# Optimization experiments

Hardware: AMD Instinct MI355X
Metric: run time of the kernel (lower is better)

Reference implementation:

```python
import jax, jax.numpy as jnp
import numpy as np

N = 100000      # nodes
E = 1600000     # edges (before self-loops)
IN_DIM = 32
HID = 64        # per-head channels of conv1
H1 = 2          # heads of conv1
OUT = 64        # conv2 out channels, heads=1
LN_EPS = 1e-5
NEG_SLOPE = 0.2   # PyG GATConv default LeakyReLU slope


def setup_inputs() -> dict:
    key = jax.random.key(0)
    ks = jax.random.split(key, 13)
    g = lambda k, shape, sc=0.1: (jax.random.normal(k, shape, jnp.float32) * sc)
    return {
        "x": jax.random.normal(ks[0], (N, IN_DIM), jnp.float32),
        "edge_index": jax.random.randint(ks[1], (2, E), 0, N, dtype=jnp.int32),
        # conv1: heads=2, out=HID -> lin weight [IN_DIM, H1*HID], att [H1, HID]
        "W1": g(ks[2], (IN_DIM, H1 * HID)),
        "att_src1": g(ks[3], (H1, HID)),
        "att_dst1": g(ks[4], (H1, HID)),
        "bias1": jnp.zeros((H1 * HID,), jnp.float32),
        # LayerNorm over 128 features
        "gamma": jnp.ones((H1 * HID,), jnp.float32),
        "beta": jnp.zeros((H1 * HID,), jnp.float32),
        # conv2: heads=1, in=128, out=OUT
        "W2": g(ks[5], (H1 * HID, OUT)),
        "att_src2": g(ks[6], (1, OUT)),
        "att_dst2": g(ks[7], (1, OUT)),
        "bias2": jnp.zeros((OUT,), jnp.float32),
    }


def gat_layer(x, src, dst, W, att_src, att_dst, bias, heads, out_ch, n):
    """PyG GATConv (shared src/dst lin, add_self_loops handled by caller)."""
    h = (x @ W).reshape(n, heads, out_ch)                 # [N,H,C]
    a_s = jnp.einsum('nhc,hc->nh', h, att_src)            # [N,H]
    a_d = jnp.einsum('nhc,hc->nh', h, att_dst)
    e = jax.nn.leaky_relu(a_s[src] + a_d[dst], NEG_SLOPE) # [E,H]
    # segment softmax over incoming edges of each destination node
    emax = jax.ops.segment_max(e, dst, num_segments=n)    # [N,H]
    e = jnp.exp(e - emax[dst])
    esum = jax.ops.segment_sum(e, dst, num_segments=n)
    alpha = e / (esum[dst] + 1e-16)                       # [E,H]
    msg = h[src] * alpha[:, :, None]                      # [E,H,C]
    out = jax.ops.segment_sum(msg, dst, num_segments=n)   # [N,H,C]
    return out.reshape(n, heads * out_ch) + bias


def reference(x, edge_index, W1, att_src1, att_dst1, bias1, gamma, beta,
              W2, att_src2, att_dst2, bias2):
    n = x.shape[0]
    loops = jnp.arange(n, dtype=edge_index.dtype)
    src = jnp.concatenate([edge_index[0], loops])         # add self-loops
    dst = jnp.concatenate([edge_index[1], loops])

    h = gat_layer(x, src, dst, W1, att_src1, att_dst1, bias1, H1, HID, n)
    # LayerNorm over feature dim, then ReLU
    mu = h.mean(-1, keepdims=True)
    var = ((h - mu) ** 2).mean(-1, keepdims=True)
    h = (h - mu) * jax.lax.rsqrt(var + LN_EPS) * gamma + beta
    h = jax.nn.relu(h)

    return gat_layer(h, src, dst, W2, att_src2, att_dst2, bias2, 1, OUT, n)
```

## Files before the change

kernel.cpp:

```cpp
#include <hip/hip_runtime.h>
#include <hip/hip_bf16.h>
#include <hip/hip_fp16.h>

#define IN_DIM 32
#define HID 64
#define H1 2
#define F1 (H1 * HID)
#define OUT_CH 64
#define NEG_SLOPE 0.2f
#define LN_EPS 1e-5f

#define BSHIFT 9
#define BMASK ((1 << BSHIFT) - 1)
#define CHUNK 4096

typedef __attribute__((ext_vector_type(8))) short short8x;
typedef __attribute__((ext_vector_type(4))) float floatx4;

__device__ __forceinline__ float leaky(float x) {
    return x > 0.f ? x : NEG_SLOPE * x;
}
__device__ __forceinline__ float bf2f(__hip_bfloat16 v) { return __bfloat162float(v); }
__device__ __forceinline__ short f2bs(float v) {
    __hip_bfloat16 t = __float2bfloat16(v);
    return *reinterpret_cast<short*>(&t);
}
__device__ __forceinline__ float unpack_w(unsigned u, int hshift) {
    return __half2float(__ushort_as_half((unsigned short)(u >> hshift)));
}


__global__ __launch_bounds__(256) void k_bhist(const int* __restrict__ dst, int E, int nb,
                                               int* __restrict__ bcnt) {
    __shared__ int h[512];
    int t = threadIdx.x;
    for (int i = t; i < nb; i += 256) h[i] = 0;
    __syncthreads();
    int base = blockIdx.x * CHUNK;
#pragma unroll
    for (int j = 0; j < 16; j++) {
        int e = base + j * 256 + t;
        if (e < E) atomicAdd(&h[dst[e] >> BSHIFT], 1);
    }
    __syncthreads();
    for (int i = t; i < nb; i += 256)
        if (h[i]) atomicAdd(&bcnt[i], h[i]);
}

__global__ __launch_bounds__(512) void k_bscan(const int* __restrict__ bcnt, int nb, int E,
                                               int* __restrict__ boff,
                                               int* __restrict__ bfill) {
    __shared__ int s[512];
    int t = threadIdx.x;
    int v = (t < nb) ? bcnt[t] : 0;
    s[t] = v;
    __syncthreads();
    for (int off = 1; off < 512; off <<= 1) {
        int u = (t >= off) ? s[t - off] : 0;
        __syncthreads();
        s[t] += u;
        __syncthreads();
    }
    if (t < nb) { int ex = s[t] - v; boff[t] = ex; bfill[t] = ex; }
    if (t == 0) boff[nb] = E;
}

__global__ __launch_bounds__(256) void k_bucket(const int* __restrict__ src,
                                                const int* __restrict__ dst, int E, int nb,
                                                int* __restrict__ bfill,
                                                unsigned int* __restrict__ bedge) {
    __shared__ int h[512];
    __shared__ int gb[512];
    int t = threadIdx.x;
    for (int i = t; i < nb; i += 256) h[i] = 0;
    __syncthreads();
    int base = blockIdx.x * CHUNK;
    unsigned int pk[16];
    int rk[16], bk[16];
#pragma unroll
    for (int j = 0; j < 16; j++) {
        int e = base + j * 256 + t;
        if (e < E) {
            int d = dst[e];
            int b = d >> BSHIFT;
            bk[j] = b;
            pk[j] = ((unsigned)src[e] << BSHIFT) | (unsigned)(d & BMASK);
            rk[j] = atomicAdd(&h[b], 1);
        } else bk[j] = -1;
    }
    __syncthreads();
    for (int i = t; i < nb; i += 256)
        gb[i] = h[i] ? atomicAdd(&bfill[i], h[i]) : 0;
    __syncthreads();
#pragma unroll
    for (int j = 0; j < 16; j++)
        if (bk[j] >= 0) bedge[gb[bk[j]] + rk[j]] = pk[j];
}

__global__ __launch_bounds__(256) void k_csr(const unsigned int* __restrict__ bedge,
                                             const int* __restrict__ boff, int n,
                                             int* __restrict__ cnt,
                                             int* __restrict__ rowptr,
                                             int* __restrict__ col) {
    int b = blockIdx.x;
    int t = threadIdx.x;
    __shared__ int lcnt[512];
    __shared__ int lscan[256];
    int nbase = b << BSHIFT;
    lcnt[2 * t] = 0; lcnt[2 * t + 1] = 0;
    __syncthreads();
    int estart = boff[b], eend = boff[b + 1];
    for (int e = estart + t; e < eend; e += 256)
        atomicAdd(&lcnt[bedge[e] & BMASK], 1);
    __syncthreads();
    int c0 = lcnt[2 * t], c1 = lcnt[2 * t + 1];
    int s = c0 + c1;
    lscan[t] = s;
    __syncthreads();
    for (int off = 1; off < 256; off <<= 1) {
        int u = (t >= off) ? lscan[t - off] : 0;
        __syncthreads();
        lscan[t] += u;
        __syncthreads();
    }
    int ex = lscan[t] - s;
    int node0 = nbase + 2 * t, node1 = node0 + 1;
    if (node0 < n) { cnt[node0] = c0; rowptr[node0] = estart + ex; }
    if (node1 < n) { cnt[node1] = c1; rowptr[node1] = estart + ex + c0; }
    __syncthreads();
    lcnt[2 * t] = ex;
    lcnt[2 * t + 1] = ex + c0;
    __syncthreads();
    for (int e = estart + t; e < eend; e += 256) {
        unsigned int p = bedge[e];
        int pos = estart + atomicAdd(&lcnt[p & BMASK], 1);
        col[pos] = (int)(p >> BSHIFT);
    }
}

__global__ __launch_bounds__(256) void k_packW(const float* __restrict__ W1,
                                               const float* __restrict__ W2,
                                               const float* __restrict__ att_s,
                                               const float* __restrict__ att_d,
                                               __hip_bfloat16* __restrict__ W1t,
                                               __hip_bfloat16* __restrict__ W2t,
                                               float* __restrict__ wsd) {
    int idx = blockIdx.x * 256 + threadIdx.x;
    if (idx < IN_DIM * F1) {
        int ch = idx >> 5, k = idx & 31;
        W1t[idx] = __float2bfloat16(W1[k * F1 + ch]);
    }
    if (idx < F1 * OUT_CH) {
        int ch = idx >> 7, k = idx & 127;
        W2t[idx] = __float2bfloat16(W2[k * OUT_CH + ch]);
    }
    if (idx < 128) {
        int v = idx >> 5;
        int k = idx & 31;
        const float* att = (v & 2) ? att_d : att_s;
        int h = v & 1;
        float s = 0.f;
#pragma unroll 8
        for (int c = 0; c < HID; c++)
            s = fmaf(W1[k * F1 + h * HID + c], att[h * HID + c], s);
        wsd[v * 32 + k] = s;
    }
}

__global__ __launch_bounds__(256) void k_att1(const float* __restrict__ x,
                                              const float* __restrict__ wsd,
                                              __hip_bfloat16* __restrict__ xb16,
                                              float2* __restrict__ as1,
                                              float2* __restrict__ ad1, int n) {
    int node = blockIdx.x * 256 + threadIdx.x;
    if (node >= n) return;
    const float4* xp = (const float4*)(x + (size_t)node * IN_DIM);
    float4 xr[8];
#pragma unroll
    for (int i = 0; i < 8; i++) xr[i] = xp[i];
    const float* xf = (const float*)xr;
    short8x* xo = (short8x*)(xb16 + (size_t)node * IN_DIM);
#pragma unroll
    for (int i = 0; i < 4; i++) {
        short8x xb;
#pragma unroll
        for (int j = 0; j < 8; j++) xb[j] = f2bs(xf[i * 8 + j]);
        xo[i] = xb;
    }
    float d0 = 0.f, d1 = 0.f, d2 = 0.f, d3 = 0.f;
#pragma unroll
    for (int k = 0; k < 32; k++) {
        float xv = xf[k];
        d0 = fmaf(xv, wsd[k], d0);
        d1 = fmaf(xv, wsd[32 + k], d1);
        d2 = fmaf(xv, wsd[64 + k], d2);
        d3 = fmaf(xv, wsd[96 + k], d3);
    }
    as1[node] = make_float2(d0, d1);
    ad1[node] = make_float2(d2, d3);
}

__global__ __launch_bounds__(256) void k_agg1x(const __hip_bfloat16* __restrict__ xb16,
                                               const float2* __restrict__ as1p,
                                               const float2* __restrict__ ad1p,
                                               const int* __restrict__ rowptr,
                                               const int* __restrict__ cnt,
                                               const int* __restrict__ col,
                                               __hip_bfloat16* __restrict__ a, int n) {
    int wave = threadIdx.x >> 6;
    int lane = threadIdx.x & 63;
    int g = lane >> 4;
    int gl = lane & 15;
    int node = blockIdx.x * 16 + wave * 4 + g;
    bool valid = node < n;
    int nc = valid ? node : 0;
    float2 adn = ad1p[nc];
    float2 asn = as1p[nc];
    const __hip_bfloat162* xv2 = (const __hip_bfloat162*)xb16;
    float w0 = __expf(leaky(asn.x + adn.x));
    float w1 = __expf(leaky(asn.y + adn.y));
    __hip_bfloat162 hv = xv2[(size_t)nc * 16 + gl];
    float x0 = bf2f(hv.x), x1 = bf2f(hv.y);
    float a00 = w0 * x0, a01 = w0 * x1;
    float a10 = w1 * x0, a11 = w1 * x1;
    float ws0 = w0, ws1 = w1;
    int start = valid ? rowptr[nc] : 0;
    int deg = valid ? cnt[nc] : 0;
    int mx = deg;
    mx = max(mx, __shfl_xor(mx, 16, 64));
    mx = max(mx, __shfl_xor(mx, 32, 64));
    int gbase = g << 4;
    for (int base = 0; base < mx; base += 16) {
        int m = deg - base;
        int colv = 0; unsigned wvv = 0u;
        if (gl < m) {
            colv = col[start + base + gl];
            float2 as = as1p[colv];
            float e0 = __expf(leaky(as.x + adn.x));
            float e1 = __expf(leaky(as.y + adn.y));
            wvv = ((unsigned)__half_as_ushort(__float2half(e1)) << 16)
                | (unsigned)__half_as_ushort(__float2half(e0));
        }
        int kend = min(16, mx - base);
        int k = 0;
        for (; k + 8 <= kend; k += 8) {
            int sx[8]; unsigned uw[8];
#pragma unroll
            for (int q = 0; q < 8; q++) {
                sx[q] = __shfl(colv, gbase + k + q);
                uw[q] = __shfl(wvv, gbase + k + q);
            }
            __hip_bfloat162 gx[8];
#pragma unroll
            for (int q = 0; q < 8; q++) gx[q] = xv2[(size_t)sx[q] * 16 + gl];
#pragma unroll
            for (int q = 0; q < 8; q++) {
                float ww0 = __half2float(__ushort_as_half((unsigned short)(uw[q] & 0xffffu)));
                float ww1 = __half2float(__ushort_as_half((unsigned short)(uw[q] >> 16)));
                float gx0 = bf2f(gx[q].x), gx1 = bf2f(gx[q].y);
                a00 = fmaf(ww0, gx0, a00); a01 = fmaf(ww0, gx1, a01);
                a10 = fmaf(ww1, gx0, a10); a11 = fmaf(ww1, gx1, a11);
                ws0 += ww0; ws1 += ww1;
            }
        }
        for (; k < kend; k++) {
            int s = __shfl(colv, gbase + k);
            unsigned u = __shfl(wvv, gbase + k);
            __hip_bfloat162 gxx = xv2[(size_t)s * 16 + gl];
            float ww0 = __half2float(__ushort_as_half((unsigned short)(u & 0xffffu)));
            float ww1 = __half2float(__ushort_as_half((unsigned short)(u >> 16)));
            float gx0 = bf2f(gxx.x), gx1 = bf2f(gxx.y);
            a00 = fmaf(ww0, gx0, a00); a01 = fmaf(ww0, gx1, a01);
            a10 = fmaf(ww1, gx0, a10); a11 = fmaf(ww1, gx1, a11);
            ws0 += ww0; ws1 += ww1;
        }
    }
    if (valid) {
        float inv0 = 1.f / (ws0 + 1e-16f);
        float inv1 = 1.f / (ws1 + 1e-16f);
        __hip_bfloat162* ao = (__hip_bfloat162*)(a + (size_t)node * 64);
        __hip_bfloat162 o0, o1;
        o0.x = __float2bfloat16(a00 * inv0); o0.y = __float2bfloat16(a01 * inv0);
        o1.x = __float2bfloat16(a10 * inv1); o1.y = __float2bfloat16(a11 * inv1);
        ao[gl] = o0;
        ao[16 + gl] = o1;
    }
}

__global__ __launch_bounds__(256) void k_ln1_mfma(const __hip_bfloat16* __restrict__ a,
                                                  const __hip_bfloat16* __restrict__ W1t,
                                                  const float* __restrict__ bias1,
                                                  const float* __restrict__ gamma,
                                                  const float* __restrict__ beta,
                                                  __hip_bfloat16* __restrict__ hlnb, int n) {
    int wave = threadIdx.x >> 6;
    int lane = threadIdx.x & 63;
    int row16 = lane & 15;
    int quad = lane >> 4;
    int node0 = blockIdx.x * 64 + wave * 16;

    short8x bfr[8];
#pragma unroll
    for (int nt = 0; nt < 8; nt++)
        bfr[nt] = *(const short8x*)(W1t + (nt * 16 + row16) * IN_DIM + quad * 8);

    int arow = node0 + row16;
    if (arow >= n) arow = n - 1;
    const __hip_bfloat16* ap = a + (size_t)arow * 64 + quad * 8;
    short8x af0 = *(const short8x*)ap;
    short8x af1 = *(const short8x*)(ap + 32);

    floatx4 acc[8];
#pragma unroll
    for (int nt = 0; nt < 8; nt++) acc[nt] = (floatx4){0.f, 0.f, 0.f, 0.f};
#pragma unroll
    for (int nt = 0; nt < 8; nt++)
        acc[nt] = __builtin_amdgcn_mfma_f32_16x16x32_bf16(nt < 4 ? af0 : af1, bfr[nt],
                                                          acc[nt], 0, 0, 0);

    float bv[8], gv[8], btv[8];
#pragma unroll
    for (int nt = 0; nt < 8; nt++) {
        int ch = nt * 16 + row16;
        bv[nt] = bias1[ch];
        gv[nt] = gamma[ch];
        btv[nt] = beta[ch];
    }
#pragma unroll
    for (int rr = 0; rr < 4; rr++) {
        int node = node0 + quad * 4 + rr;
        float v[8];
        float sum = 0.f, sq = 0.f;
#pragma unroll
        for (int nt = 0; nt < 8; nt++) {
            v[nt] = acc[nt][rr] + bv[nt];
            sum += v[nt];
            sq += v[nt] * v[nt];
        }
#pragma unroll
        for (int off = 1; off < 16; off <<= 1) {
            sum += __shfl_xor(sum, off, 64);
            sq += __shfl_xor(sq, off, 64);
        }
        float mu = sum * (1.f / 128.f);
        float var = sq * (1.f / 128.f) - mu * mu;
        float r = rsqrtf(var + LN_EPS);
        if (node < n) {
#pragma unroll
            for (int nt = 0; nt < 8; nt++) {
                float o = (v[nt] - mu) * r * gv[nt] + btv[nt];
                hlnb[(size_t)node * F1 + nt * 16 + row16] = __float2bfloat16(fmaxf(o, 0.f));
            }
        }
    }
}

__global__ __launch_bounds__(256) void k_node2_mfma(const __hip_bfloat16* __restrict__ hlnb,
                                                    const __hip_bfloat16* __restrict__ W2t,
                                                    const float* __restrict__ att_s2,
                                                    const float* __restrict__ att_d2,
                                                    __hip_bfloat16* __restrict__ h2b,
                                                    float* __restrict__ as2,
                                                    float* __restrict__ ad2, int n) {
    int wave = threadIdx.x >> 6;
    int lane = threadIdx.x & 63;
    int row16 = lane & 15;
    int quad = lane >> 4;
    int node0 = blockIdx.x * 64 + wave * 16;

    short8x bfr[4][4];
#pragma unroll
    for (int nt = 0; nt < 4; nt++) {
        const __hip_bfloat16* wrow = W2t + (nt * 16 + row16) * F1 + quad * 8;
#pragma unroll
        for (int kc = 0; kc < 4; kc++)
            bfr[kc][nt] = *(const short8x*)(wrow + kc * 32);
    }

    floatx4 acc[4];
#pragma unroll
    for (int nt = 0; nt < 4; nt++) acc[nt] = (floatx4){0.f, 0.f, 0.f, 0.f};

    int arow = node0 + row16;
    if (arow >= n) arow = n - 1;
    const __hip_bfloat16* aptr = hlnb + (size_t)arow * F1 + quad * 8;
#pragma unroll
    for (int kc = 0; kc < 4; kc++) {
        short8x af = *(const short8x*)(aptr + kc * 32);
#pragma unroll
        for (int nt = 0; nt < 4; nt++)
            acc[nt] = __builtin_amdgcn_mfma_f32_16x16x32_bf16(af, bfr[kc][nt], acc[nt], 0, 0, 0);
    }

    float asv[4], adv[4];
#pragma unroll
    for (int nt = 0; nt < 4; nt++) {
        asv[nt] = att_s2[nt * 16 + row16];
        adv[nt] = att_d2[nt * 16 + row16];
    }
#pragma unroll
    for (int rr = 0; rr < 4; rr++) {
        int node = node0 + quad * 4 + rr;
        float ps = 0.f, pd = 0.f;
#pragma unroll
        for (int nt = 0; nt < 4; nt++) {
            float v = acc[nt][rr];
            if (node < n) h2b[(size_t)node * OUT_CH + nt * 16 + row16] = __float2bfloat16(v);
            ps = fmaf(v, asv[nt], ps);
            pd = fmaf(v, adv[nt], pd);
        }
#pragma unroll
        for (int off = 1; off < 16; off <<= 1) {
            ps += __shfl_xor(ps, off, 64);
            pd += __shfl_xor(pd, off, 64);
        }
        if (row16 == 0 && node < n) { as2[node] = ps; ad2[node] = pd; }
    }
}

__global__ __launch_bounds__(256) void k_agg2(const __hip_bfloat162* __restrict__ h2b2,
                                              const float* __restrict__ as2,
                                              const float* __restrict__ ad2,
                                              const int* __restrict__ rowptr,
                                              const int* __restrict__ cnt,
                                              const int* __restrict__ col,
                                              const float* __restrict__ bias2,
                                              float* __restrict__ out, int n) {
    int node = blockIdx.x * 4 + (threadIdx.x >> 6);
    int lane = threadIdx.x & 63;
    if (node >= n) return;
    int hl = lane & 31;
    int half = lane >> 5;
    float adn = ad2[node];
    float w = __expf(leaky(as2[node] + adn));
    __hip_bfloat162 hv = h2b2[(size_t)node * 32 + hl];
    float acc0 = half ? 0.f : w * bf2f(hv.x);
    float acc1 = half ? 0.f : w * bf2f(hv.y);
    float wsum = half ? 0.f : w;
    int start = rowptr[node], deg = cnt[node];
    for (int base = 0; base < deg; base += 64) {
        int m = min(64, deg - base);
        int colv = 0; float wvv = 0.f;
        if (lane < m) {
            colv = col[start + base + lane];
            wvv = __expf(leaky(as2[colv] + adn));
        }
        int P = (m + 1) >> 1;
        int p = 0;
        for (; p + 8 <= P; p += 8) {
            int sx[8]; float wx[8];
#pragma unroll
            for (int q = 0; q < 8; q++) {
                int k = 2 * (p + q) + half;
                sx[q] = __shfl(colv, k);
                wx[q] = __shfl(wvv, k);
            }
            __hip_bfloat162 gx[8];
#pragma unroll
            for (int q = 0; q < 8; q++) gx[q] = h2b2[(size_t)sx[q] * 32 + hl];
#pragma unroll
            for (int q = 0; q < 8; q++) {
                acc0 = fmaf(wx[q], bf2f(gx[q].x), acc0);
                acc1 = fmaf(wx[q], bf2f(gx[q].y), acc1);
                wsum += wx[q];
            }
        }
        for (; p < P; p++) {
            int k = 2 * p + half;
            int s = __shfl(colv, k);
            float wk = __shfl(wvv, k);
            __hip_bfloat162 g = h2b2[(size_t)s * 32 + hl];
            acc0 = fmaf(wk, bf2f(g.x), acc0);
            acc1 = fmaf(wk, bf2f(g.y), acc1);
            wsum += wk;
        }
    }
    acc0 += __shfl_xor(acc0, 32, 64);
    acc1 += __shfl_xor(acc1, 32, 64);
    wsum += __shfl_xor(wsum, 32, 64);
    float inv = 1.f / (wsum + 1e-16f);
    if (half == 0) {
        float2 bv = ((const float2*)bias2)[hl];
        float2 ov;
        ov.x = acc0 * inv + bv.x;
        ov.y = acc1 * inv + bv.y;
        ((float2*)out)[(size_t)node * 32 + hl] = ov;
    }
}

extern "C" void kernel_launch(void* const* d_in, const int* in_sizes, int n_in,
                              void* d_out, int out_size, void* d_ws, size_t ws_size,
                              hipStream_t stream) {
    const float* x        = (const float*)d_in[0];
    const int*   eidx     = (const int*)d_in[1];
    const float* W1       = (const float*)d_in[2];
    const float* att_src1 = (const float*)d_in[3];
    const float* att_dst1 = (const float*)d_in[4];
    const float* bias1    = (const float*)d_in[5];
    const float* gamma    = (const float*)d_in[6];
    const float* beta     = (const float*)d_in[7];
    const float* W2       = (const float*)d_in[8];
    const float* att_src2 = (const float*)d_in[9];
    const float* att_dst2 = (const float*)d_in[10];
    const float* bias2    = (const float*)d_in[11];
    float* out = (float*)d_out;

    const int N = in_sizes[0] / IN_DIM;
    const int E = in_sizes[1] / 2;
    const int* src = eidx;
    const int* dst = eidx + E;
    const int nb = (N + BMASK) >> BSHIFT;

    char* w = (char*)d_ws;
    __hip_bfloat16* xb16  = (__hip_bfloat16*)w;  w += (size_t)N * IN_DIM * 2;
    __hip_bfloat16* a     = (__hip_bfloat16*)w;  w += (size_t)N * 64 * 2;
    __hip_bfloat16* hlnb  = (__hip_bfloat16*)w;  w += (size_t)N * F1 * 2;
    __hip_bfloat16* h2b   = (__hip_bfloat16*)w;  w += (size_t)N * OUT_CH * 2;
    __hip_bfloat16* W1t   = (__hip_bfloat16*)w;  w += IN_DIM * F1 * 2;
    __hip_bfloat16* W2t   = (__hip_bfloat16*)w;  w += F1 * OUT_CH * 2;
    float* wsd = (float*)w; w += 128 * 4;
    float* as1 = (float*)w; w += (size_t)N * 2 * 4;
    float* ad1 = (float*)w; w += (size_t)N * 2 * 4;
    float* as2 = (float*)w; w += (size_t)N * 4;
    float* ad2 = (float*)w; w += (size_t)N * 4;
    int* cnt    = (int*)w; w += (size_t)N * 4;
    int* rowptr = (int*)w; w += (size_t)N * 4;
    int* bcnt   = (int*)w; w += 512 * 4;
    int* boff   = (int*)w; w += 520 * 4;
    int* bfill  = (int*)w; w += 512 * 4;
    int* col    = (int*)w; w += (size_t)E * 4;
    unsigned int* bedge = (unsigned int*)w; w += (size_t)E * 4;

    const int nchunk = (E + CHUNK - 1) / CHUNK;

    hipMemsetAsync(bcnt, 0, 512 * 4, stream);
    k_bhist<<<nchunk, 256, 0, stream>>>(dst, E, nb, bcnt);
    k_bscan<<<1, 512, 0, stream>>>(bcnt, nb, E, boff, bfill);
    k_bucket<<<nchunk, 256, 0, stream>>>(src, dst, E, nb, bfill, bedge);
    k_csr<<<nb, 256, 0, stream>>>(bedge, boff, N, cnt, rowptr, col);

    k_packW<<<(F1 * OUT_CH + 255) / 256, 256, 0, stream>>>(W1, W2, att_src1, att_dst1,
                                                           W1t, W2t, wsd);
    k_att1<<<(N + 255) / 256, 256, 0, stream>>>(x, wsd, xb16,
                                                (float2*)as1, (float2*)ad1, N);
    k_agg1x<<<(N + 15) / 16, 256, 0, stream>>>(xb16, (const float2*)as1, (const float2*)ad1,
                                               rowptr, cnt, col, a, N);
    k_ln1_mfma<<<(N + 63) / 64, 256, 0, stream>>>(a, W1t, bias1, gamma, beta, hlnb, N);

    k_node2_mfma<<<(N + 63) / 64, 256, 0, stream>>>(hlnb, W2t, att_src2, att_dst2,
                                                    h2b, as2, ad2, N);
    k_agg2<<<(N + 3) / 4, 256, 0, stream>>>((const __hip_bfloat162*)h2b, as2, ad2,
                                            rowptr, cnt, col, bias2, out, N);
}
```

Before: 279.4 us.

## Stage edge index/weights in LDS and use packed FMA in GAT aggregation kernels

```diff
diff --git a/kernel.cpp b/kernel.cpp
--- a/kernel.cpp
+++ b/kernel.cpp
@@ -16,6 +16,7 @@
 
 typedef __attribute__((ext_vector_type(8))) short short8x;
 typedef __attribute__((ext_vector_type(4))) float floatx4;
+typedef __attribute__((ext_vector_type(2))) float floatx2;
 
 __device__ __forceinline__ float leaky(float x) {
     return x > 0.f ? x : NEG_SLOPE * x;
@@ -25,8 +26,11 @@
     __hip_bfloat16 t = __float2bfloat16(v);
     return *reinterpret_cast<short*>(&t);
 }
-__device__ __forceinline__ float unpack_w(unsigned u, int hshift) {
-    return __half2float(__ushort_as_half((unsigned short)(u >> hshift)));
+__device__ __forceinline__ void pk_fma(floatx2& c, floatx2 a, floatx2 b) {
+    asm("v_pk_fma_f32 %0, %1, %2, %0" : "+v"(c) : "v"(a), "v"(b));
+}
+__device__ __forceinline__ void lds_fence() {
+    asm volatile("s_waitcnt lgkmcnt(0)" ::: "memory");
 }
 
 
@@ -207,6 +211,7 @@
                                                const int* __restrict__ cnt,
                                                const int* __restrict__ col,
                                                __hip_bfloat16* __restrict__ a, int n) {
+    __shared__ float4 est[4][64];
     int wave = threadIdx.x >> 6;
     int lane = threadIdx.x & 63;
     int g = lane >> 4;
@@ -216,13 +221,14 @@
     int nc = valid ? node : 0;
     float2 adn = ad1p[nc];
     float2 asn = as1p[nc];
-    const __hip_bfloat162* xv2 = (const __hip_bfloat162*)xb16;
+    const unsigned* xu = (const unsigned*)xb16;
     float w0 = __expf(leaky(asn.x + adn.x));
     float w1 = __expf(leaky(asn.y + adn.y));
-    __hip_bfloat162 hv = xv2[(size_t)nc * 16 + gl];
-    float x0 = bf2f(hv.x), x1 = bf2f(hv.y);
-    float a00 = w0 * x0, a01 = w0 * x1;
-    float a10 = w1 * x0, a11 = w1 * x1;
+    unsigned su = xu[(size_t)nc * 16 + gl];
+    float x0 = __uint_as_float(su << 16);
+    float x1 = __uint_as_float(su & 0xffff0000u);
+    floatx2 accA = {w0 * x0, w1 * x0};
+    floatx2 accB = {w0 * x1, w1 * x1};
     float ws0 = w0, ws1 = w1;
     int start = valid ? rowptr[nc] : 0;
     int deg = valid ? cnt[nc] : 0;
@@ -232,47 +238,53 @@
     int gbase = g << 4;
     for (int base = 0; base < mx; base += 16) {
         int m = deg - base;
-        int colv = 0; unsigned wvv = 0u;
+        float e0 = 0.f, e1 = 0.f; int cv = 0;
         if (gl < m) {
-            colv = col[start + base + gl];
-            float2 as = as1p[colv];
-            float e0 = __expf(leaky(as.x + adn.x));
-            float e1 = __expf(leaky(as.y + adn.y));
-            wvv = ((unsigned)__half_as_ushort(__float2half(e1)) << 16)
-                | (unsigned)__half_as_ushort(__float2half(e0));
-        }
+            cv = col[start + base + gl];
+            float2 as = as1p[cv];
+            e0 = __expf(leaky(as.x + adn.x));
+            e1 = __expf(leaky(as.y + adn.y));
+        }
+        lds_fence();
+        float4 e; e.x = __int_as_float(cv); e.y = 0.f; e.z = e0; e.w = e1;
+        est[wave][lane] = e;
+        float r0 = e0, r1 = e1;
+#pragma unroll
+        for (int off = 1; off < 16; off <<= 1) {
+            r0 += __shfl_xor(r0, off, 64);
+            r1 += __shfl_xor(r1, off, 64);
+        }
+        ws0 += r0; ws1 += r1;
+        lds_fence();
         int kend = min(16, mx - base);
         int k = 0;
         for (; k + 8 <= kend; k += 8) {
-            int sx[8]; unsigned uw[8];
+            float4 ef[8];
+#pragma unroll
+            for (int q = 0; q < 8; q++) ef[q] = est[wave][gbase + k + q];
+            unsigned gu[8];
+#pragma unroll
+            for (int q = 0; q < 8; q++)
+                gu[q] = xu[(size_t)__float_as_int(ef[q].x) * 16 + gl];
 #pragma unroll
             for (int q = 0; q < 8; q++) {
-                sx[q] = __shfl(colv, gbase + k + q);
-                uw[q] = __shfl(wvv, gbase + k + q);
+                floatx2 wp = {ef[q].z, ef[q].w};
+                float glo = __uint_as_float(gu[q] << 16);
+                float ghi = __uint_as_float(gu[q] & 0xffff0000u);
+                floatx2 gA = {glo, glo}, gB = {ghi, ghi};
+                pk_fma(accA, wp, gA);
+                pk_fma(accB, wp, gB);
             }
-            __hip_bfloat162 gx[8];
-#pragma unroll
-            for (int q = 0; q < 8; q++) gx[q] = xv2[(size_t)sx[q] * 16 + gl];
-#pragma unroll
-            for (int q = 0; q < 8; q++) {
-                float ww0 = __half2float(__ushort_as_half((unsigned short)(uw[q] & 0xffffu)));
-                float ww1 = __half2float(__ushort_as_half((unsigned short)(uw[q] >> 16)));
-                float gx0 = bf2f(gx[q].x), gx1 = bf2f(gx[q].y);
-                a00 = fmaf(ww0, gx0, a00); a01 = fmaf(ww0, gx1, a01);
-                a10 = fmaf(ww1, gx0, a10); a11 = fmaf(ww1, gx1, a11);
-                ws0 += ww0; ws1 += ww1;
-            }
         }
         for (; k < kend; k++) {
-            int s = __shfl(colv, gbase + k);
-            unsigned u = __shfl(wvv, gbase + k);
-            __hip_bfloat162 gxx = xv2[(size_t)s * 16 + gl];
-            float ww0 = __half2float(__ushort_as_half((unsigned short)(u & 0xffffu)));
-            float ww1 = __half2float(__ushort_as_half((unsigned short)(u >> 16)));
-            float gx0 = bf2f(gxx.x), gx1 = bf2f(gxx.y);
-            a00 = fmaf(ww0, gx0, a00); a01 = fmaf(ww0, gx1, a01);
-            a10 = fmaf(ww1, gx0, a10); a11 = fmaf(ww1, gx1, a11);
-            ws0 += ww0; ws1 += ww1;
+            float4 ef = est[wave][gbase + k];
+            unsigned u = xu[(size_t)__float_as_int(ef.x) * 16 + gl];
+            floatx2 wp = {ef.z, ef.w};
+            float glo = __uint_as_float(u << 16);
+            float ghi = __uint_as_float(u & 0xffff0000u);
+            floatx2 gA = {glo, glo}, gB = {ghi, ghi};
+            pk_fma(accA, wp, gA);
+            pk_fma(accB, wp, gB);
         }
     }
     if (valid) {
@@ -280,8 +292,8 @@
         float inv1 = 1.f / (ws1 + 1e-16f);
         __hip_bfloat162* ao = (__hip_bfloat162*)(a + (size_t)node * 64);
         __hip_bfloat162 o0, o1;
-        o0.x = __float2bfloat16(a00 * inv0); o0.y = __float2bfloat16(a01 * inv0);
-        o1.x = __float2bfloat16(a10 * inv1); o1.y = __float2bfloat16(a11 * inv1);
+        o0.x = __float2bfloat16(accA.x * inv0); o0.y = __float2bfloat16(accB.x * inv0);
+        o1.x = __float2bfloat16(accA.y * inv1); o1.y = __float2bfloat16(accB.y * inv1);
         ao[gl] = o0;
         ao[16 + gl] = o1;
     }
@@ -426,64 +438,72 @@
                                               const int* __restrict__ col,
                                               const float* __restrict__ bias2,
                                               float* __restrict__ out, int n) {
-    int node = blockIdx.x * 4 + (threadIdx.x >> 6);
+    __shared__ float4 est[4][64];
+    int wave = threadIdx.x >> 6;
     int lane = threadIdx.x & 63;
+    int node = blockIdx.x * 4 + wave;
     if (node >= n) return;
     int hl = lane & 31;
     int half = lane >> 5;
+    const unsigned* h2u = (const unsigned*)h2b2;
     float adn = ad2[node];
-    float w = __expf(leaky(as2[node] + adn));
-    __hip_bfloat162 hv = h2b2[(size_t)node * 32 + hl];
-    float acc0 = half ? 0.f : w * bf2f(hv.x);
-    float acc1 = half ? 0.f : w * bf2f(hv.y);
-    float wsum = half ? 0.f : w;
+    float wself = __expf(leaky(as2[node] + adn));
+    unsigned su = h2u[(size_t)node * 32 + hl];
+    float sx0 = __uint_as_float(su << 16);
+    float sx1 = __uint_as_float(su & 0xffff0000u);
+    floatx2 acc = {half ? 0.f : wself * sx0, half ? 0.f : wself * sx1};
+    float wsum = wself;
     int start = rowptr[node], deg = cnt[node];
     for (int base = 0; base < deg; base += 64) {
         int m = min(64, deg - base);
-        int colv = 0; float wvv = 0.f;
+        float wv = 0.f; int cv = 0;
         if (lane < m) {
-            colv = col[start + base + lane];
-            wvv = __expf(leaky(as2[colv] + adn));
-        }
+            cv = col[start + base + lane];
+            wv = __expf(leaky(as2[cv] + adn));
+        }
+        lds_fence();
+        float4 e; e.x = __int_as_float(cv); e.y = 0.f; e.z = wv; e.w = wv;
+        est[wave][lane] = e;
+        float r = wv;
+#pragma unroll
+        for (int off = 1; off < 64; off <<= 1) r += __shfl_xor(r, off, 64);
+        wsum += r;
+        lds_fence();
         int P = (m + 1) >> 1;
         int p = 0;
         for (; p + 8 <= P; p += 8) {
-            int sx[8]; float wx[8];
+            float4 ef[8];
+#pragma unroll
+            for (int q = 0; q < 8; q++) ef[q] = est[wave][2 * (p + q) + half];
+            unsigned gu[8];
+#pragma unroll
+            for (int q = 0; q < 8; q++)
+                gu[q] = h2u[(size_t)__float_as_int(ef[q].x) * 32 + hl];
 #pragma unroll
             for (int q = 0; q < 8; q++) {
-                int k = 2 * (p + q) + half;
-                sx[q] = __shfl(colv, k);
-                wx[q] = __shfl(wvv, k);
+                floatx2 wp = {ef[q].z, ef[q].w};
+                floatx2 g = {__uint_as_float(gu[q] << 16),
+                             __uint_as_float(gu[q] & 0xffff0000u)};
+                pk_fma(acc, wp, g);
             }
-            __hip_bfloat162 gx[8];
-#pragma unroll
-            for (int q = 0; q < 8; q++) gx[q] = h2b2[(size_t)sx[q] * 32 + hl];
-#pragma unroll
-            for (int q = 0; q < 8; q++) {
-                acc0 = fmaf(wx[q], bf2f(gx[q].x), acc0);
-                acc1 = fmaf(wx[q], bf2f(gx[q].y), acc1);
-                wsum += wx[q];
-            }
         }
         for (; p < P; p++) {
-            int k = 2 * p + half;
-            int s = __shfl(colv, k);
-            float wk = __shfl(wvv, k);
-            __hip_bfloat162 g = h2b2[(size_t)s * 32 + hl];
-            acc0 = fmaf(wk, bf2f(g.x), acc0);
-            acc1 = fmaf(wk, bf2f(g.y), acc1);
-            wsum += wk;
-        }
-    }
-    acc0 += __shfl_xor(acc0, 32, 64);
-    acc1 += __shfl_xor(acc1, 32, 64);
-    wsum += __shfl_xor(wsum, 32, 64);
+            float4 ef = est[wave][2 * p + half];
+            unsigned u = h2u[(size_t)__float_as_int(ef.x) * 32 + hl];
+            floatx2 wp = {ef.z, ef.w};
+            floatx2 g = {__uint_as_float(u << 16),
+                         __uint_as_float(u & 0xffff0000u)};
+            pk_fma(acc, wp, g);
+        }
+    }
+    float a0 = acc.x + __shfl_xor(acc.x, 32, 64);
+    float a1 = acc.y + __shfl_xor(acc.y, 32, 64);
     float inv = 1.f / (wsum + 1e-16f);
     if (half == 0) {
         float2 bv = ((const float2*)bias2)[hl];
         float2 ov;
-        ov.x = acc0 * inv + bv.x;
-        ov.y = acc1 * inv + bv.y;
+        ov.x = a0 * inv + bv.x;
+        ov.y = a1 * inv + bv.y;
         ((float2*)out)[(size_t)node * 32 + hl] = ov;
     }
 }
```

After: 291.5 us. 1.04x slower.
